# Optimization experiments

Hardware: AMD Instinct MI355X
Metric: run time of the kernel (lower is better)

Reference implementation:

```python
import jax, jax.numpy as jnp
from jax import lax
import numpy as np

K = 3          # kernel_size
PAD = 1        # K // 2
MAX_OFFSET = 0.1
EPS = 1e-8


def setup_inputs() -> dict:
    key = jax.random.key(0)
    k0, k1, k2 = jax.random.split(key, 3)
    B, C, H, W = 4, 64, 256, 256
    Cmid = C // 4
    x = jax.random.normal(k0, (B, C, H, W), jnp.float32)
    # offset_predictor: Conv2d(C+9, C//4, 3, pad=1) -> LeakyReLU(0.2) -> Conv2d(C//4, 2, 3, pad=1) -> Tanh
    w1 = jax.random.normal(k1, (Cmid, C + K * K, 3, 3), jnp.float32) * 0.05
    b1 = jnp.zeros((Cmid,), jnp.float32)
    w2 = jax.random.normal(k2, (2, Cmid, 3, 3), jnp.float32) * 0.05
    b2 = jnp.zeros((2,), jnp.float32)
    return {"x": x, "w1": w1, "b1": b1, "w2": w2, "b2": b2}


def _conv2d(x, w, b):
    # NCHW, OIHW, stride 1, pad 1 (SAME for 3x3)
    out = lax.conv_general_dilated(x, w, (1, 1), ((PAD, PAD), (PAD, PAD)),
                                   dimension_numbers=("NCHW", "OIHW", "NCHW"))
    return out + b[None, :, None, None]


def _local_cosine_similarity(x):
    # F.unfold with zero padding: neighbors[k] at spatial shift (di-1, dj-1), row-major k = di*K + dj
    B, C, H, W = x.shape
    xp = jnp.pad(x, ((0, 0), (0, 0), (PAD, PAD), (PAD, PAD)))
    neighbors = jnp.stack([xp[:, :, di:di + H, dj:dj + W]
                           for di in range(K) for dj in range(K)], axis=2)  # (B,C,9,H,W)
    center = x[:, :, None, :, :]                                            # (B,C,1,H,W)
    numerator = jnp.sum(neighbors * center, axis=1)                         # (B,9,H,W)
    center_norm = jnp.sqrt(jnp.sum(x * x, axis=1)) + EPS                    # (B,H,W)
    neighbor_norm = jnp.sqrt(jnp.sum(neighbors * neighbors, axis=1)) + EPS  # (B,9,H,W)
    return numerator / (center_norm[:, None] * neighbor_norm)               # (B,9,H,W)


def _grid_sample_border(x, grid):
    # bilinear, padding_mode='border', align_corners=True; grid: (B,H,W,2) with (gx,gy) in [-1,1]
    B, C, H, W = x.shape
    ix = (grid[..., 0] + 1.0) * 0.5 * (W - 1)
    iy = (grid[..., 1] + 1.0) * 0.5 * (H - 1)
    ix = jnp.clip(ix, 0.0, W - 1)
    iy = jnp.clip(iy, 0.0, H - 1)
    x0f = jnp.floor(ix); y0f = jnp.floor(iy)
    wx = ix - x0f; wy = iy - y0f
    x0 = x0f.astype(jnp.int32); y0 = y0f.astype(jnp.int32)
    x1 = jnp.minimum(x0 + 1, W - 1); y1 = jnp.minimum(y0 + 1, H - 1)

    def gather(img, yy, xx):  # img (C,H,W), yy/xx (H,W) -> (C,H,W)
        return img[:, yy, xx]

    g = jax.vmap(gather)
    v00 = g(x, y0, x0); v01 = g(x, y0, x1)
    v10 = g(x, y1, x0); v11 = g(x, y1, x1)
    wx = wx[:, None]; wy = wy[:, None]  # broadcast over channel dim
    return ((1 - wy) * ((1 - wx) * v00 + wx * v01)
            + wy * ((1 - wx) * v10 + wx * v11))


def reference(x, w1, b1, w2, b2):
    B, C, H, W = x.shape
    sim = _local_cosine_similarity(x)                       # (B,9,H,W)
    features = jnp.concatenate([x, sim], axis=1)            # (B,C+9,H,W)
    h = _conv2d(features, w1, b1)
    h = jnp.where(h >= 0, h, 0.2 * h)                       # LeakyReLU(0.2)
    offset = jnp.tanh(_conv2d(h, w2, b2)) * MAX_OFFSET      # (B,2,H,W)
    gy, gx = jnp.meshgrid(jnp.linspace(-1.0, 1.0, H),
                          jnp.linspace(-1.0, 1.0, W), indexing="ij")
    base_grid = jnp.stack([gx, gy], axis=-1)[None]          # (1,H,W,2)
    offset_grid = base_grid + jnp.transpose(offset, (0, 2, 3, 1))
    return _grid_sample_border(x, offset_grid)
```

## Files before the change

kernel.cpp:

```cpp
#include <hip/hip_runtime.h>
#include <math.h>

#define B 4
#define C 64
#define H 256
#define W 256
#define CMID 16
#define CIN 73
#define HW (H*W)
#define NW (CIN*9*CMID)
#define XS_STRIDE 260

__global__ void transpose_w1_kernel(const float* __restrict__ w1, float* __restrict__ wt) {
    int tid = blockIdx.x * blockDim.x + threadIdx.x;
    if (tid >= NW) return;
    int co = tid & (CMID - 1);
    int rest = tid >> 4;
    int ci = rest / 9;
    int k = rest - ci * 9;
    wt[tid] = w1[(co * CIN + ci) * 9 + k];
}


__device__ __forceinline__ void read_patch9(const float* __restrict__ base, float v[9]) {
#pragma unroll
    for (int r = 0; r < 3; ++r) {
        v[r * 3 + 0] = base[r * XS_STRIDE + 0];
        v[r * 3 + 1] = base[r * XS_STRIDE + 1];
        v[r * 3 + 2] = base[r * XS_STRIDE + 2];
    }
}

__device__ __forceinline__ void zero_halo48(float* __restrict__ xs0, int tid) {
    if (tid < 48) {
        int e = tid & 1;
        int r = (tid >> 1) % 3;
        int q = (tid >> 1) / 3;
        xs0[q * (3 * XS_STRIDE) + r * XS_STRIDE + (e ? 257 : 0)] = 0.f;
    }
}

__global__ __launch_bounds__(256) void sim_kernel(const float* __restrict__ x,
                                                  float* __restrict__ sim) {
    __shared__ float xs[2][4][3 * XS_STRIDE];

    int bid = blockIdx.x;
    int b = bid >> 8;
    int y = bid & 255;
    int tid = threadIdx.x;

    const float* xb = x + (size_t)b * C * HW;

    bool rv[3];
    long off[3];
#pragma unroll
    for (int j = 0; j < 3; ++j) {
        int grow = y - 1 + j;
        rv[j] = (grow >= 0) && (grow < H);
        off[j] = (long)grow * W + tid;
    }

    zero_halo48(&xs[0][0][0], tid);

    float dot[9], nsq[9];
    float csq = 0.f;
#pragma unroll
    for (int i = 0; i < 9; ++i) { dot[i] = nsq[i] = 0.f; }

    float p[12];
#pragma unroll
    for (int k = 0; k < 4; ++k)
#pragma unroll
        for (int j = 0; j < 3; ++j)
            p[k * 3 + j] = rv[j] ? xb[(size_t)k * HW + off[j]] : 0.f;

    int cur = 0;
#pragma unroll 1
    for (int cc = 0; cc < C; cc += 4) {
#pragma unroll
        for (int k = 0; k < 4; ++k)
#pragma unroll
            for (int j = 0; j < 3; ++j)
                xs[cur][k][j * XS_STRIDE + 1 + tid] = p[k * 3 + j];
        __syncthreads();

        if (cc + 4 < C) {
#pragma unroll
            for (int k = 0; k < 4; ++k)
#pragma unroll
                for (int j = 0; j < 3; ++j)
                    p[k * 3 + j] = rv[j] ? xb[(size_t)(cc + 4 + k) * HW + off[j]] : 0.f;
        }

#pragma unroll
        for (int k = 0; k < 4; ++k) {
            float v[9];
            read_patch9(&xs[cur][k][tid], v);
            float cv = v[4];
            csq = fmaf(cv, cv, csq);
#pragma unroll
            for (int kk = 0; kk < 9; ++kk) {
                if (kk == 4) continue;
                dot[kk] = fmaf(cv, v[kk], dot[kk]);
                nsq[kk] = fmaf(v[kk], v[kk], nsq[kk]);
            }
        }
        cur ^= 1;
    }

    dot[4] = csq;
    nsq[4] = csq;
    float cn = sqrtf(csq) + 1e-8f;
    float* so = sim + (size_t)b * 9 * HW + (size_t)y * W + tid;
#pragma unroll
    for (int kk = 0; kk < 9; ++kk)
        so[(size_t)kk * HW] = dot[kk] / (cn * (sqrtf(nsq[kk]) + 1e-8f));
}

__device__ __forceinline__ void conv1_chan1(const float* __restrict__ base,
                                            const float* __restrict__ wp,
                                            float acc[CMID]) {
    float v[9];
    read_patch9(base, v);
#pragma unroll
    for (int k = 0; k < 9; ++k) {
        const float* w = wp + k * CMID;
        float a = v[k];
#pragma unroll
        for (int co = 0; co < CMID; ++co)
            acc[co] = fmaf(a, w[co], acc[co]);
    }
}

__global__ __launch_bounds__(256) void conv1_kernel(const float* __restrict__ x,
                                                    const float* __restrict__ sim,
                                                    const float* __restrict__ wt,
                                                    const float* __restrict__ b1,
                                                    float* __restrict__ h) {
    __shared__ float xs[2][4][3 * XS_STRIDE];

    int bid = blockIdx.x;
    int b = bid >> 8;
    int y = bid & 255;
    int tid = threadIdx.x;

    const float* gx = x + (size_t)b * C * HW;
    const float* gs = sim + (size_t)b * 9 * HW;

    bool rv[3];
    long off[3];
#pragma unroll
    for (int j = 0; j < 3; ++j) {
        int grow = y - 1 + j;
        rv[j] = (grow >= 0) && (grow < H);
        off[j] = (long)grow * W + tid;
    }

    zero_halo48(&xs[0][0][0], tid);

    float acc[CMID];
#pragma unroll
    for (int co = 0; co < CMID; ++co) acc[co] = b1[co];

    float p[12];
#pragma unroll
    for (int k = 0; k < 4; ++k)
#pragma unroll
        for (int j = 0; j < 3; ++j)
            p[k * 3 + j] = rv[j] ? gx[(size_t)k * HW + off[j]] : 0.f;

    int cur = 0;
#pragma unroll 1
    for (int cc = 0; cc < 72; cc += 4) {
#pragma unroll
        for (int k = 0; k < 4; ++k)
#pragma unroll
            for (int j = 0; j < 3; ++j)
                xs[cur][k][j * XS_STRIDE + 1 + tid] = p[k * 3 + j];
        __syncthreads();

#pragma unroll
        for (int k = 0; k < 4; ++k) {
            int ci = cc + 4 + k;
            if (ci < CIN) {
                const float* cb = (ci < C) ? (gx + (size_t)ci * HW)
                                           : (gs + (size_t)(ci - C) * HW);
#pragma unroll
                for (int j = 0; j < 3; ++j)
                    p[k * 3 + j] = rv[j] ? cb[off[j]] : 0.f;
            }
        }

        conv1_chan1(&xs[cur][0][tid], wt + (size_t)cc * 144, acc);
        conv1_chan1(&xs[cur][1][tid], wt + (size_t)(cc + 1) * 144, acc);
        conv1_chan1(&xs[cur][2][tid], wt + (size_t)(cc + 2) * 144, acc);
        conv1_chan1(&xs[cur][3][tid], wt + (size_t)(cc + 3) * 144, acc);
        cur ^= 1;
    }

#pragma unroll
    for (int j = 0; j < 3; ++j)
        xs[cur][0][j * XS_STRIDE + 1 + tid] = p[j];
    __syncthreads();
    conv1_chan1(&xs[cur][0][tid], wt + (size_t)72 * 144, acc);

    float* ho = h + (size_t)b * CMID * HW + (size_t)y * W + tid;
#pragma unroll
    for (int co = 0; co < CMID; ++co) {
        float v0 = acc[co];
        v0 = v0 >= 0.f ? v0 : 0.2f * v0;
        ho[(size_t)co * HW] = v0;
    }
}

__device__ __forceinline__ void read_patch_lds(const float* __restrict__ xsbuf,
                                               int rl, int px, float v[3][4]) {
    const float* pb = xsbuf + rl * XS_STRIDE + px;
#pragma unroll
    for (int r = 0; r < 3; ++r) {
        float2 p0 = *(const float2*)(pb + r * XS_STRIDE);
        float2 p1 = *(const float2*)(pb + r * XS_STRIDE + 2);
        v[r][0] = p0.x; v[r][1] = p0.y; v[r][2] = p1.x; v[r][3] = p1.y;
    }
}

__global__ __launch_bounds__(256) void offset_kernel(const float* __restrict__ h,
                                                     const float* __restrict__ w2,
                                                     const float* __restrict__ b2,
                                                     float2* __restrict__ off_buf) {
    __shared__ float lw2[CMID * 9 * 2];
    __shared__ float xs[2][4 * XS_STRIDE];

    int tid = threadIdx.x;
    for (int i = tid; i < CMID * 9 * 2; i += 256) {
        int co = i & 1;
        int rest = i >> 1;
        int ci = rest / 9;
        int kk = rest - ci * 9;
        lw2[i] = w2[(co * CMID + ci) * 9 + kk];
    }

    int bid = blockIdx.x;
    int b  = bid >> 7;
    int y0 = (bid & 127) << 1;
    int srow = tid >> 6;
    int sx4  = (tid & 63) << 2;
    int rl = tid >> 7;
    int px = (tid & 127) << 1;
    int y  = y0 + rl;

    int grow = y0 - 1 + srow;
    bool gvalid = (grow >= 0) && (grow < H);
    const float* gh = h + (size_t)b * CMID * HW + (size_t)grow * W + sx4;

    if (tid < 16) {
        int bu = tid >> 3, r = (tid >> 1) & 3, e = (tid & 1) ? 257 : 0;
        xs[bu][r * XS_STRIDE + e] = 0.f;
    }

    float s0x = b2[0], s0y = b2[1], s1x = b2[0], s1y = b2[1];

    float4 r4 = make_float4(0.f, 0.f, 0.f, 0.f);
    if (gvalid) r4 = *(const float4*)gh;

    int cur = 0;
#pragma unroll 1
    for (int ci = 0; ci < CMID; ++ci) {
        float* dst = &xs[cur][srow * XS_STRIDE + 1 + sx4];
        dst[0] = r4.x; dst[1] = r4.y; dst[2] = r4.z; dst[3] = r4.w;
        __syncthreads();
        if (ci + 1 < CMID) {
            r4 = make_float4(0.f, 0.f, 0.f, 0.f);
            if (gvalid) r4 = *(const float4*)(gh + (size_t)(ci + 1) * HW);
        }
        float v[3][4];
        read_patch_lds(xs[cur], rl, px, v);
#pragma unroll
        for (int kr = 0; kr < 3; ++kr)
#pragma unroll
            for (int kc = 0; kc < 3; ++kc) {
                float2 wv = *(const float2*)(lw2 + (ci * 9 + kr * 3 + kc) * 2);
                s0x = fmaf(v[kr][kc],     wv.x, s0x);
                s0y = fmaf(v[kr][kc],     wv.y, s0y);
                s1x = fmaf(v[kr][kc + 1], wv.x, s1x);
                s1y = fmaf(v[kr][kc + 1], wv.y, s1y);
            }
        cur ^= 1;
    }

    float ix0 = (float)px       + 0.1f * tanhf(s0x) * (0.5f * (float)(W - 1));
    float iy0 = (float)y        + 0.1f * tanhf(s0y) * (0.5f * (float)(H - 1));
    float ix1 = (float)(px + 1) + 0.1f * tanhf(s1x) * (0.5f * (float)(W - 1));
    float iy1 = (float)y        + 0.1f * tanhf(s1y) * (0.5f * (float)(H - 1));
    ix0 = fminf(fmaxf(ix0, 0.f), (float)(W - 1));
    iy0 = fminf(fmaxf(iy0, 0.f), (float)(H - 1));
    ix1 = fminf(fmaxf(ix1, 0.f), (float)(W - 1));
    iy1 = fminf(fmaxf(iy1, 0.f), (float)(H - 1));

    float4* op = (float4*)(off_buf + (size_t)b * HW + (size_t)y * W + px);
    *op = make_float4(ix0, iy0, ix1, iy1);
}

#define SROWS 35
__global__ __launch_bounds__(256) void sample_kernel(const float* __restrict__ x,
                                                     const float2* __restrict__ off_buf,
                                                     float* __restrict__ out) {
    __shared__ float xs[SROWS * 256];

    int bid = blockIdx.x;
    int sb = (bid & 7) * 16 + (bid >> 3);
    int b  = sb >> 5;
    int ty = sb & 31;
    int cg = blockIdx.y;
    int tid = threadIdx.x;

    int ybase = ty << 3;
    int lo = ybase - 13;

    int a00[8], a01[8], a10[8], a11[8];
    float wx[8], wy[8];
    const float2* ob2 = off_buf + (size_t)b * HW + (size_t)ybase * W + tid;
#pragma unroll
    for (int r = 0; r < 8; ++r) {
        float2 o = ob2[r * W];
        float xf = floorf(o.x), yf = floorf(o.y);
        wx[r] = o.x - xf; wy[r] = o.y - yf;
        int x0 = (int)xf, yy0 = (int)yf;
        int x1 = min(x0 + 1, W - 1), yy1 = min(yy0 + 1, H - 1);
        int r0 = (yy0 - lo) << 8, r1 = (yy1 - lo) << 8;
        a00[r] = r0 + x0; a01[r] = r0 + x1;
        a10[r] = r1 + x0; a11[r] = r1 + x1;
    }

    const float* xb = x + ((size_t)b * C + cg * 4) * HW;
    float* outb = out + ((size_t)b * C + cg * 4) * HW + (size_t)ybase * W + tid;

#pragma unroll 1
    for (int c = 0; c < 4; ++c) {
        __syncthreads();
        const float* src = xb + (size_t)c * HW;
        for (int j = tid; j < SROWS * 64; j += 256) {
            int row = j >> 6, x4 = (j & 63) << 2;
            int grw = min(max(lo + row, 0), H - 1);
            *(float4*)&xs[(row << 8) + x4] = *(const float4*)(src + (size_t)grw * W + x4);
        }
        __syncthreads();
        float* oc = outb + (size_t)c * HW;
#pragma unroll
        for (int r = 0; r < 8; ++r) {
            float v00 = xs[a00[r]], v01 = xs[a01[r]];
            float v10 = xs[a10[r]], v11 = xs[a11[r]];
            float top = fmaf(wx[r], v01 - v00, v00);
            float bot = fmaf(wx[r], v11 - v10, v10);
            oc[r * W] = fmaf(wy[r], bot - top, top);
        }
    }
}

extern "C" void kernel_launch(void* const* d_in, const int* in_sizes, int n_in,
                              void* d_out, int out_size, void* d_ws, size_t ws_size,
                              hipStream_t stream) {
    const float* x  = (const float*)d_in[0];
    const float* w1 = (const float*)d_in[1];
    const float* b1 = (const float*)d_in[2];
    const float* w2 = (const float*)d_in[3];
    const float* b2 = (const float*)d_in[4];
    float* out = (float*)d_out;

    float* ws  = (float*)d_ws;
    float* wt  = ws;
    float* sim = ws + 16384;
    float* h   = sim + (size_t)B * 9 * HW;
    float2* off_buf = (float2*)(h + (size_t)B * CMID * HW);

    transpose_w1_kernel<<<(NW + 255) / 256, 256, 0, stream>>>(w1, wt);

    sim_kernel<<<B * H, 256, 0, stream>>>(x, sim);
    conv1_kernel<<<B * H, 256, 0, stream>>>(x, sim, wt, b1, h);
    offset_kernel<<<512, 256, 0, stream>>>(h, w2, b2, off_buf);
    sample_kernel<<<dim3(128, 16), 256, 0, stream>>>(x, off_buf, out);
}
```

Before: 256.6 us.

## Stage conv1 weights in LDS, swizzle block order, shrink channel tiles

conv1 now copies the full transposed weight tensor (about 42 KB) into shared memory and reads it as float4 broadcasts instead of scalar global loads. Its channel staging drops from a double-buffered 4-channel tile to a single-buffered 2-channel tile with an extra barrier per iteration. The LDS row stride shrinks from 260 to 258. All three kernels remap block IDs so that consecutive blocks are spread across the eight XCDs, which is meant to improve cache locality. The large LDS footprint lowers occupancy for conv1, and the extra barriers reduce the overlap between loads and compute.

Result: slower. 276.4 us (+7.7%).

```diff
diff --git a/kernel.cpp b/kernel.cpp
--- a/kernel.cpp
+++ b/kernel.cpp
@@ -10,6 +10,7 @@
 #define HW (H*W)
 #define NW (CIN*9*CMID)
 #define XS_STRIDE 260
+#define XSR 258
 
 __global__ void transpose_w1_kernel(const float* __restrict__ w1, float* __restrict__ wt) {
     int tid = blockIdx.x * blockDim.x + threadIdx.x;
@@ -21,46 +22,42 @@
     wt[tid] = w1[(co * CIN + ci) * 9 + k];
 }
 
-
 __device__ __forceinline__ void read_patch9(const float* __restrict__ base, float v[9]) {
 #pragma unroll
     for (int r = 0; r < 3; ++r) {
-        v[r * 3 + 0] = base[r * XS_STRIDE + 0];
-        v[r * 3 + 1] = base[r * XS_STRIDE + 1];
-        v[r * 3 + 2] = base[r * XS_STRIDE + 2];
-    }
-}
-
-__device__ __forceinline__ void zero_halo48(float* __restrict__ xs0, int tid) {
+        v[r * 3 + 0] = base[r * XSR + 0];
+        v[r * 3 + 1] = base[r * XSR + 1];
+        v[r * 3 + 2] = base[r * XSR + 2];
+    }
+}
+
+__global__ __launch_bounds__(256) void sim_kernel(const float* __restrict__ x,
+                                                  float* __restrict__ sim) {
+    __shared__ float xs[2][4][3 * XSR];
+
+    int bid = blockIdx.x;
+    int sb = (bid & 7) * 128 + (bid >> 3);
+    int b = sb >> 8;
+    int y = sb & 255;
+    int tid = threadIdx.x;
+
+    const float* xb = x + (size_t)b * C * HW;
+
+    bool rv[3];
+    long off[3];
+#pragma unroll
+    for (int j = 0; j < 3; ++j) {
+        int grow = y - 1 + j;
+        rv[j] = (grow >= 0) && (grow < H);
+        off[j] = (long)grow * W + tid;
+    }
+
     if (tid < 48) {
         int e = tid & 1;
         int r = (tid >> 1) % 3;
         int q = (tid >> 1) / 3;
-        xs0[q * (3 * XS_STRIDE) + r * XS_STRIDE + (e ? 257 : 0)] = 0.f;
-    }
-}
-
-__global__ __launch_bounds__(256) void sim_kernel(const float* __restrict__ x,
-                                                  float* __restrict__ sim) {
-    __shared__ float xs[2][4][3 * XS_STRIDE];
-
-    int bid = blockIdx.x;
-    int b = bid >> 8;
-    int y = bid & 255;
-    int tid = threadIdx.x;
-
-    const float* xb = x + (size_t)b * C * HW;
-
-    bool rv[3];
-    long off[3];
-#pragma unroll
-    for (int j = 0; j < 3; ++j) {
-        int grow = y - 1 + j;
-        rv[j] = (grow >= 0) && (grow < H);
-        off[j] = (long)grow * W + tid;
-    }
-
-    zero_halo48(&xs[0][0][0], tid);
+        (&xs[0][0][0])[q * (3 * XSR) + r * XSR + (e ? 257 : 0)] = 0.f;
+    }
 
     float dot[9], nsq[9];
     float csq = 0.f;
@@ -81,7 +78,7 @@
         for (int k = 0; k < 4; ++k)
 #pragma unroll
             for (int j = 0; j < 3; ++j)
-                xs[cur][k][j * XS_STRIDE + 1 + tid] = p[k * 3 + j];
+                xs[cur][k][j * XSR + 1 + tid] = p[k * 3 + j];
         __syncthreads();
 
         if (cc + 4 < C) {
@@ -118,17 +115,23 @@
 }
 
 __device__ __forceinline__ void conv1_chan1(const float* __restrict__ base,
-                                            const float* __restrict__ wp,
+                                            const float* __restrict__ wch,
                                             float acc[CMID]) {
     float v[9];
     read_patch9(base, v);
 #pragma unroll
     for (int k = 0; k < 9; ++k) {
-        const float* w = wp + k * CMID;
+        const float4* w4 = (const float4*)(wch + k * CMID);
         float a = v[k];
-#pragma unroll
-        for (int co = 0; co < CMID; ++co)
-            acc[co] = fmaf(a, w[co], acc[co]);
+        float4 w0 = w4[0], w1 = w4[1], w2 = w4[2], w3 = w4[3];
+        acc[0]  = fmaf(a, w0.x, acc[0]);  acc[1]  = fmaf(a, w0.y, acc[1]);
+        acc[2]  = fmaf(a, w0.z, acc[2]);  acc[3]  = fmaf(a, w0.w, acc[3]);
+        acc[4]  = fmaf(a, w1.x, acc[4]);  acc[5]  = fmaf(a, w1.y, acc[5]);
+        acc[6]  = fmaf(a, w1.z, acc[6]);  acc[7]  = fmaf(a, w1.w, acc[7]);
+        acc[8]  = fmaf(a, w2.x, acc[8]);  acc[9]  = fmaf(a, w2.y, acc[9]);
+        acc[10] = fmaf(a, w2.z, acc[10]); acc[11] = fmaf(a, w2.w, acc[11]);
+        acc[12] = fmaf(a, w3.x, acc[12]); acc[13] = fmaf(a, w3.y, acc[13]);
+        acc[14] = fmaf(a, w3.z, acc[14]); acc[15] = fmaf(a, w3.w, acc[15]);
     }
 }
 
@@ -137,12 +140,18 @@
                                                     const float* __restrict__ wt,
                                                     const float* __restrict__ b1,
                                                     float* __restrict__ h) {
-    __shared__ float xs[2][4][3 * XS_STRIDE];
-
+    __shared__ float lw[NW];
+    __shared__ float xs[2][3 * XSR];
+
+    int tid = threadIdx.x;
     int bid = blockIdx.x;
-    int b = bid >> 8;
-    int y = bid & 255;
-    int tid = threadIdx.x;
+    int sb = (bid & 7) * 128 + (bid >> 3);
+    int b = sb >> 8;
+    int y = sb & 255;
+
+#pragma unroll 1
+    for (int j = tid; j < NW / 4; j += 256)
+        ((float4*)lw)[j] = ((const float4*)wt)[j];
 
     const float* gx = x + (size_t)b * C * HW;
     const float* gs = sim + (size_t)b * 9 * HW;
@@ -156,32 +165,36 @@
         off[j] = (long)grow * W + tid;
     }
 
-    zero_halo48(&xs[0][0][0], tid);
+    if (tid < 12) {
+        int e = tid & 1;
+        int r = (tid >> 1) % 3;
+        int ch = (tid >> 1) / 3;
+        xs[ch][r * XSR + (e ? 257 : 0)] = 0.f;
+    }
 
     float acc[CMID];
 #pragma unroll
     for (int co = 0; co < CMID; ++co) acc[co] = b1[co];
 
-    float p[12];
-#pragma unroll
-    for (int k = 0; k < 4; ++k)
+    float p[6];
+#pragma unroll
+    for (int k = 0; k < 2; ++k)
 #pragma unroll
         for (int j = 0; j < 3; ++j)
             p[k * 3 + j] = rv[j] ? gx[(size_t)k * HW + off[j]] : 0.f;
 
-    int cur = 0;
-#pragma unroll 1
-    for (int cc = 0; cc < 72; cc += 4) {
-#pragma unroll
-        for (int k = 0; k < 4; ++k)
+#pragma unroll 1
+    for (int cc = 0; cc < 72; cc += 2) {
+#pragma unroll
+        for (int k = 0; k < 2; ++k)
 #pragma unroll
             for (int j = 0; j < 3; ++j)
-                xs[cur][k][j * XS_STRIDE + 1 + tid] = p[k * 3 + j];
-        __syncthreads();
-
-#pragma unroll
-        for (int k = 0; k < 4; ++k) {
-            int ci = cc + 4 + k;
+                xs[k][j * XSR + 1 + tid] = p[k * 3 + j];
+        __syncthreads();
+
+#pragma unroll
+        for (int k = 0; k < 2; ++k) {
+            int ci = cc + 2 + k;
             if (ci < CIN) {
                 const float* cb = (ci < C) ? (gx + (size_t)ci * HW)
                                            : (gs + (size_t)(ci - C) * HW);
@@ -191,18 +204,16 @@
             }
         }
 
-        conv1_chan1(&xs[cur][0][tid], wt + (size_t)cc * 144, acc);
-        conv1_chan1(&xs[cur][1][tid], wt + (size_t)(cc + 1) * 144, acc);
-        conv1_chan1(&xs[cur][2][tid], wt + (size_t)(cc + 2) * 144, acc);
-        conv1_chan1(&xs[cur][3][tid], wt + (size_t)(cc + 3) * 144, acc);
-        cur ^= 1;
+        conv1_chan1(&xs[0][tid], lw + (size_t)cc * 144, acc);
+        conv1_chan1(&xs[1][tid], lw + (size_t)(cc + 1) * 144, acc);
+        __syncthreads();
     }
 
 #pragma unroll
     for (int j = 0; j < 3; ++j)
-        xs[cur][0][j * XS_STRIDE + 1 + tid] = p[j];
+        xs[0][j * XSR + 1 + tid] = p[j];
     __syncthreads();
-    conv1_chan1(&xs[cur][0][tid], wt + (size_t)72 * 144, acc);
+    conv1_chan1(&xs[0][tid], lw + (size_t)72 * 144, acc);
 
     float* ho = h + (size_t)b * CMID * HW + (size_t)y * W + tid;
 #pragma unroll
@@ -241,8 +252,9 @@
     }
 
     int bid = blockIdx.x;
-    int b  = bid >> 7;
-    int y0 = (bid & 127) << 1;
+    int sb = (bid & 7) * 64 + (bid >> 3);
+    int b  = sb >> 7;
+    int y0 = (sb & 127) << 1;
     int srow = tid >> 6;
     int sx4  = (tid & 63) << 2;
     int rl = tid >> 7;
```
